# Kernel optimization log

Hardware: AMD Instinct MI355X
Metric: run time of the kernel (lower is better)

The kernel has to match this reference:

```python
import jax, jax.numpy as jnp
import numpy as np

DEGREE = 3          # bspline_array passes t_dim positionally as degree
C_DIM = 64          # coefficients per spline
N_SPLINES = 64      # n
T_DIM = C_DIM + DEGREE + 1   # knots per spline = 68
BATCH = 65536


def setup_inputs() -> dict:
    key = jax.random.key(0)
    k1, k2, k3 = jax.random.split(key, 3)
    x = jax.random.normal(k1, (BATCH, N_SPLINES), dtype=jnp.float32)
    t = jax.random.normal(k2, (N_SPLINES, T_DIM), dtype=jnp.float32)   # knot vectors (learned, unsorted as in source)
    c = jax.random.normal(k3, (N_SPLINES, C_DIM), dtype=jnp.float32)   # control coefficients
    return {"x": x, "t": t, "c": c}


def _safe_div(num, den):
    # Cox-de Boor convention: 0/0 := 0 (handles repeated knots)
    zero = den == 0
    return jnp.where(zero, 0.0, num / jnp.where(zero, 1.0, den))


def cox_deboor_batched(t, c, x):
    """Vectorized Cox-de Boor over all n splines and the whole batch.

    t: [n, T_DIM] knots, c: [n, C_DIM] coeffs, x: [B, n] -> out [B, n]
    """
    xe = x[..., None]                                   # [B, n, 1]
    # degree-0 basis: indicator t_i <= x < t_{i+1}      # [B, n, T_DIM-1]
    N = ((t[:, :-1] <= xe) & (xe < t[:, 1:])).astype(x.dtype)
    for k in range(1, DEGREE + 1):
        m = T_DIM - 1 - k
        left = _safe_div(xe - t[:, :m], t[:, k:k + m] - t[:, :m]) * N[..., :m]
        right = _safe_div(t[:, k + 1:k + 1 + m] - xe,
                          t[:, k + 1:k + 1 + m] - t[:, 1:1 + m]) * N[..., 1:1 + m]
        N = left + right                                # [B, n, m]
    # S(x) = sum_i c_i * B_{i,p}(x)
    return jnp.einsum('bni,ni->bn', N[..., :C_DIM], c)  # [B, n]


def reference(x, t, c):
    return cox_deboor_batched(t, c, x)
```

## Files before the change

### kernel.cpp

```cpp
#include <hip/hip_runtime.h>

#define BATCH 65536
#define NSPL  64
#define CDIM  64
#define TDIM  68
#define QI    67
#define RTN   67

#define TCOLS 16
#define TROWS 128
#define NTHR  256
#define KPAD  128
#define KLDS  132


__global__ __launch_bounds__(128) void prep(const float* __restrict__ T,
                                            const float* __restrict__ C,
                                            float4* __restrict__ RT,
                                            float* __restrict__ SRT) {
    __shared__ double  td[TDIM];
    __shared__ double  cd[CDIM];
    __shared__ double  R1[QI], R2[TDIM - 2], R3[TDIM - 3];
    __shared__ double4 Qd[QI];
    __shared__ float   tf[TDIM];
    __shared__ float   srt[TDIM];

    const int s = blockIdx.x;
    const int t = threadIdx.x;

    if (t < TDIM) { float v = T[s * TDIM + t]; tf[t] = v; td[t] = (double)v; }
    if (t >= 64 && t < 64 + CDIM) cd[t - 64] = (double)C[s * CDIM + t - 64];
    __syncthreads();

    if (t < TDIM - 1) { double d = td[t + 1] - td[t]; R1[t] = (d == 0.0) ? 0.0 : 1.0 / d; }
    if (t < TDIM - 2) { double d = td[t + 2] - td[t]; R2[t] = (d == 0.0) ? 0.0 : 1.0 / d; }
    if (t < TDIM - 3) { double d = td[t + 3] - td[t]; R3[t] = (d == 0.0) ? 0.0 : 1.0 / d; }
    if (t < TDIM) {
        float v = tf[t];
        int r = 0;
        for (int k = 0; k < TDIM; ++k)
            r += (tf[k] < v) || (tf[k] == v && k < t);
        srt[r] = v;
    }
    __syncthreads();

    {
        float v = (t < TDIM) ? srt[t] : __builtin_huge_valf();
        SRT[s * KPAD + t] = v;
    }

    if (t < QI) {
        const int i = t;
        double q0 = 0, q1 = 0, q2 = 0, q3 = 0;
        for (int j = i - 3; j <= i; ++j) {
            if (j < 0 || j > CDIM - 1) continue;
            double cj = cd[j];
            for (int b2 = 0; b2 < 2; ++b2) {
                int m2 = j + b2;
                double D3 = R3[j + b2];
                double p3 = b2 ? -D3 : D3;
                double r3 = b2 ? D3 * td[j + 4] : -D3 * td[j];
                for (int b1 = 0; b1 < 2; ++b1) {
                    int m1 = m2 + b1;
                    double D2 = R2[m2 + b1];
                    double p2 = b1 ? -D2 : D2;
                    double r2 = b1 ? D2 * td[m2 + 3] : -D2 * td[m2];
                    for (int b0 = 0; b0 < 2; ++b0) {
                        if (m1 + b0 != i) continue;
                        double D1 = R1[m1 + b0];
                        double p1 = b0 ? -D1 : D1;
                        double r1 = b0 ? D1 * td[m1 + 2] : -D1 * td[m1];
                        double a2 = p3 * p2, a1 = p3 * r2 + r3 * p2, a0 = r3 * r2;
                        q3 += cj * (a2 * p1);
                        q2 += cj * (a2 * r1 + a1 * p1);
                        q1 += cj * (a1 * r1 + a0 * p1);
                        q0 += cj * (a0 * r1);
                    }
                }
            }
        }
        double4 q; q.x = q0; q.y = q1; q.z = q2; q.w = q3;
        Qd[i] = q;
    }
    __syncthreads();

    if (t >= 1 && t <= RTN) {
        const float xs = srt[t - 1];
        double a0 = 0, a1 = 0, a2 = 0, a3 = 0;
        for (int i = 0; i < QI; ++i) {
            if (tf[i] <= xs && xs < tf[i + 1]) {
                double4 q = Qd[i];
                a0 += q.x; a1 += q.y; a2 += q.z; a3 += q.w;
            }
        }
        float4 v; v.x = (float)a0; v.y = (float)a1; v.z = (float)a2; v.w = (float)a3;
        RT[s * RTN + (t - 1)] = v;
    }
}

__global__ __launch_bounds__(NTHR, 8) void bspline_main(const float* __restrict__ X,
                                                        const float4* __restrict__ RT,
                                                        const float* __restrict__ SRT,
                                                        float* __restrict__ O) {
    __shared__ float ks[TCOLS * KLDS];

    const int tid = threadIdx.x;
    const int r0  = blockIdx.x * TROWS;
    const int s0  = blockIdx.y * TCOLS;

    {
        const float4* src = (const float4*)(SRT + s0 * KPAD);
        #pragma unroll
        for (int it = 0; it < 2; ++it) {
            int e = tid + it * NTHR;
            int c = e >> 5, p = e & 31;
            float4 v = src[c * 32 + p];
            *(float4*)(ks + c * KLDS + p * 4) = v;
        }
    }
    __syncthreads();

    const int c  = tid & 15;
    const int rs = tid >> 4;
    const float* kc = ks + c * KLDS;

    const float pv1  = kc[63];
    const float pv2a = kc[31], pv2b = kc[95];
    const float pv3a = kc[15], pv3b = kc[47], pv3c = kc[79], pv3d = kc[111];

    const float4* rts = RT + (s0 + c) * RTN;
    const float*  xp  = X + (r0 + rs) * NSPL + s0 + c;
    float*        op  = O + (r0 + rs) * NSPL + s0 + c;

    #pragma unroll
    for (int j = 0; j < 4; ++j) {
        const int ra = (32 * j) * NSPL, rb = (32 * j + 16) * NSPL;
        const float x0 = xp[ra];
        const float x1 = xp[rb];

        unsigned n0 = (pv1 <= x0) ? 64u : 0u;
        unsigned n1 = (pv1 <= x1) ? 64u : 0u;
        float q0 = n0 ? pv2b : pv2a;
        float q1 = n1 ? pv2b : pv2a;
        n0 += (q0 <= x0) ? 32u : 0u;
        n1 += (q1 <= x1) ? 32u : 0u;
        float a0 = (n0 & 32u) ? pv3b : pv3a;
        float b0 = (n0 & 32u) ? pv3d : pv3c;
        float a1 = (n1 & 32u) ? pv3b : pv3a;
        float b1 = (n1 & 32u) ? pv3d : pv3c;
        float r0v = (n0 & 64u) ? b0 : a0;
        float r1v = (n1 & 64u) ? b1 : a1;
        n0 += (r0v <= x0) ? 16u : 0u;
        n1 += (r1v <= x1) ? 16u : 0u;
        #pragma unroll
        for (int st = 8; st >= 1; st >>= 1) {
            float v0 = kc[n0 + st - 1];
            float v1 = kc[n1 + st - 1];
            n0 = (v0 <= x0) ? n0 + st : n0;
            n1 = (v1 <= x1) ? n1 + st : n1;
        }

        unsigned i0 = n0 - 1u; i0 = (i0 > 66u) ? 66u : i0;
        unsigned i1 = n1 - 1u; i1 = (i1 > 66u) ? 66u : i1;
        float4 p0 = rts[i0];
        float4 p1 = rts[i1];
        float y0 = fmaf(fmaf(fmaf(p0.w, x0, p0.z), x0, p0.y), x0, p0.x);
        float y1 = fmaf(fmaf(fmaf(p1.w, x1, p1.z), x1, p1.y), x1, p1.x);
        y0 = (n0 - 1u < 67u) ? y0 : 0.f;
        y1 = (n1 - 1u < 67u) ? y1 : 0.f;
        op[ra] = y0;
        op[rb] = y1;
    }
}

extern "C" void kernel_launch(void* const* d_in, const int* in_sizes, int n_in,
                              void* d_out, int out_size, void* d_ws, size_t ws_size,
                              hipStream_t stream) {
    const float* X = (const float*)d_in[0];
    const float* T = (const float*)d_in[1];
    const float* C = (const float*)d_in[2];
    float* O = (float*)d_out;
    float4* RT = (float4*)d_ws;
    float* SRT = (float*)((char*)d_ws + NSPL * RTN * sizeof(float4));

    prep<<<NSPL, 128, 0, stream>>>(T, C, RT, SRT);
    dim3 grid(BATCH / TROWS, NSPL / TCOLS);
    bspline_main<<<grid, NTHR, 0, stream>>>(X, RT, SRT, O);
}
```

Before: 88.32 us.

## Vectorize X/O access with float4 per thread covering four splines

Each thread now handles four adjacent spline columns for one row, so X is loaded and O stored as float4 instead of scalar accesses. The thread-to-data mapping changes from 16 columns by 16 rows to 4 column quads by 64 rows. The third-level pivot registers are dropped and the search uses one more LDS-probed binary step, trading some LDS reads for fewer registers. The point is fewer, wider global memory instructions, at the cost of more LDS bank pressure, because the four columns handled by a thread sit on different LDS rows.

```diff
diff --git a/kernel.cpp b/kernel.cpp
--- a/kernel.cpp
+++ b/kernel.cpp
@@ -120,56 +120,52 @@
     }
     __syncthreads();
 
-    const int c  = tid & 15;
-    const int rs = tid >> 4;
-    const float* kc = ks + c * KLDS;
+    const int q  = tid & 3;
+    const int rs = tid >> 2;
+    const int c0 = q * 4;
 
-    const float pv1  = kc[63];
-    const float pv2a = kc[31], pv2b = kc[95];
-    const float pv3a = kc[15], pv3b = kc[47], pv3c = kc[79], pv3d = kc[111];
+    float pv1[4], pv2a[4], pv2b[4];
+    #pragma unroll
+    for (int cc = 0; cc < 4; ++cc) {
+        const float* kc = ks + (c0 + cc) * KLDS;
+        pv1[cc]  = kc[63];
+        pv2a[cc] = kc[31];
+        pv2b[cc] = kc[95];
+    }
 
-    const float4* rts = RT + (s0 + c) * RTN;
-    const float*  xp  = X + (r0 + rs) * NSPL + s0 + c;
-    float*        op  = O + (r0 + rs) * NSPL + s0 + c;
+    const float4* xp = (const float4*)(X + (r0 + rs) * NSPL + s0) + q;
+    float4*       op = (float4*)(O + (r0 + rs) * NSPL + s0) + q;
+    const int rstride = NSPL / 4;
 
     #pragma unroll
-    for (int j = 0; j < 4; ++j) {
-        const int ra = (32 * j) * NSPL, rb = (32 * j + 16) * NSPL;
-        const float x0 = xp[ra];
-        const float x1 = xp[rb];
+    for (int h = 0; h < 2; ++h) {
+        const int roff = h * 64 * rstride;
+        const float4 xv = xp[roff];
+        float y[4];
+        const float xs[4] = { xv.x, xv.y, xv.z, xv.w };
 
-        unsigned n0 = (pv1 <= x0) ? 64u : 0u;
-        unsigned n1 = (pv1 <= x1) ? 64u : 0u;
-        float q0 = n0 ? pv2b : pv2a;
-        float q1 = n1 ? pv2b : pv2a;
-        n0 += (q0 <= x0) ? 32u : 0u;
-        n1 += (q1 <= x1) ? 32u : 0u;
-        float a0 = (n0 & 32u) ? pv3b : pv3a;
-        float b0 = (n0 & 32u) ? pv3d : pv3c;
-        float a1 = (n1 & 32u) ? pv3b : pv3a;
-        float b1 = (n1 & 32u) ? pv3d : pv3c;
-        float r0v = (n0 & 64u) ? b0 : a0;
-        float r1v = (n1 & 64u) ? b1 : a1;
-        n0 += (r0v <= x0) ? 16u : 0u;
-        n1 += (r1v <= x1) ? 16u : 0u;
         #pragma unroll
-        for (int st = 8; st >= 1; st >>= 1) {
-            float v0 = kc[n0 + st - 1];
-            float v1 = kc[n1 + st - 1];
-            n0 = (v0 <= x0) ? n0 + st : n0;
-            n1 = (v1 <= x1) ? n1 + st : n1;
+        for (int cc = 0; cc < 4; ++cc) {
+            const float x = xs[cc];
+            const float* kc = ks + (c0 + cc) * KLDS;
+
+            unsigned n = (pv1[cc] <= x) ? 64u : 0u;
+            float t2 = n ? pv2b[cc] : pv2a[cc];
+            n += (t2 <= x) ? 32u : 0u;
+            #pragma unroll
+            for (int st = 16; st >= 1; st >>= 1) {
+                float v = kc[n + st - 1];
+                n = (v <= x) ? n + st : n;
+            }
+
+            unsigned i = n - 1u; i = (i > 66u) ? 66u : i;
+            float4 p = RT[(s0 + c0 + cc) * RTN + i];
+            float yy = fmaf(fmaf(fmaf(p.w, x, p.z), x, p.y), x, p.x);
+            y[cc] = (n - 1u < 67u) ? yy : 0.f;
         }
 
-        unsigned i0 = n0 - 1u; i0 = (i0 > 66u) ? 66u : i0;
-        unsigned i1 = n1 - 1u; i1 = (i1 > 66u) ? 66u : i1;
-        float4 p0 = rts[i0];
-        float4 p1 = rts[i1];
-        float y0 = fmaf(fmaf(fmaf(p0.w, x0, p0.z), x0, p0.y), x0, p0.x);
-        float y1 = fmaf(fmaf(fmaf(p1.w, x1, p1.z), x1, p1.y), x1, p1.x);
-        y0 = (n0 - 1u < 67u) ? y0 : 0.f;
-        y1 = (n1 - 1u < 67u) ? y1 : 0.f;
-        op[ra] = y0;
-        op[rb] = y1;
+        float4 yv; yv.x = y[0]; yv.y = y[1]; yv.z = y[2]; yv.w = y[3];
+        op[roff] = yv;
     }
 }
 
```

After: 90.36 us. +2.3%, slower.
